# Optimization experiments

Hardware: AMD Instinct MI355X
Metric: run time of the kernel (lower is better)

Reference implementation:

```python
import jax, jax.numpy as jnp
import numpy as np

K = 64


def setup_inputs() -> dict:
    key = jax.random.key(0)
    k1, k2, k3, k4, k5 = jax.random.split(key, 5)
    B, D, F = 8192, 2048, 16384
    x = jax.random.normal(k1, (B, D), dtype=jnp.float32)
    W_enc = jax.random.normal(k2, (D, F), dtype=jnp.float32) * (1.0 / np.sqrt(D))
    b_enc = jax.random.normal(k3, (F,), dtype=jnp.float32) * 0.01
    W_dec = jax.random.normal(k4, (F, D), dtype=jnp.float32) * (1.0 / np.sqrt(F))
    b_dec = jax.random.normal(k5, (D,), dtype=jnp.float32) * 0.01
    return {"x": x, "W_enc": W_enc, "b_enc": b_enc, "W_dec": W_dec, "b_dec": b_dec}


def reference(x, W_enc, b_enc, W_dec, b_dec):
    # encode: dense GEMM + bias + relu -> [B, F]
    z = jax.nn.relu(x @ W_enc + b_enc)
    # top-k masking: keep only the k largest activations per row
    vals, idx = jax.lax.top_k(z, K)                     # [B, K]
    B = z.shape[0]
    rows = jnp.arange(B)[:, None]                       # [B, 1]
    sparse_z = jnp.zeros_like(z).at[rows, idx].set(vals)  # scatter back to [B, F]
    # decode: GEMM on k-sparse activations + bias -> [B, D]
    recon = sparse_z @ W_dec + b_dec
    return recon
```

## Files before the change

kernel.cpp:

```cpp
#include <hip/hip_runtime.h>
#include <hip/hip_bf16.h>
#include <stdint.h>

#define TK 64
#define FDIM 16384
#define DDIM 2048
#define NCAP 128
#define CCAP 384
#define SLOTS 12
#define TCAND 2.25f

typedef __attribute__((ext_vector_type(8))) short bf16x8;
typedef __attribute__((ext_vector_type(4))) float f32x4;

#define GLL(g, p)                                                        \
  __builtin_amdgcn_global_load_lds(                                      \
      (const __attribute__((address_space(1))) uint32_t*)(g),            \
      (__attribute__((address_space(3))) uint32_t*)(p), 16, 0, 0)

__device__ __forceinline__ unsigned short f2bf(float a) {
  union { float f; uint32_t u; } p; p.f = a;
  uint32_t u = p.u;
  return (unsigned short)((u + 0x7FFFu + ((u >> 16) & 1u)) >> 16);
}
__device__ __forceinline__ float bf2f(unsigned short h) {
  union { uint32_t u; float f; } p; p.u = ((uint32_t)h) << 16; return p.f;
}

__global__ __launch_bounds__(256) void conv_x(
    const float* __restrict__ x, unsigned short* __restrict__ xh, int n4)
{
  int i = blockIdx.x * 256 + threadIdx.x;
  const int stride = gridDim.x * 256;
  for (; i < n4; i += stride) {
    float4 v = ((const float4*)x)[i];
    ushort4 h;
    h.x = f2bf(v.x); h.y = f2bf(v.y); h.z = f2bf(v.z); h.w = f2bf(v.w);
    ((ushort4*)xh)[i] = h;
  }
}

__global__ __launch_bounds__(256) void conv_w(
    const float* __restrict__ W, float* __restrict__ wtf,
    unsigned short* __restrict__ wh)
{
  __shared__ float t[32][33];
  const int f0 = blockIdx.x * 32, d0 = blockIdx.y * 32;
  const int tr = threadIdx.x >> 3;
  const int tc = (threadIdx.x & 7) * 4;
  float4 v = *(const float4*)(W + (size_t)(d0 + tr) * FDIM + f0 + tc);
  t[tr][tc + 0] = v.x; t[tr][tc + 1] = v.y;
  t[tr][tc + 2] = v.z; t[tr][tc + 3] = v.w;
  __syncthreads();
  float a0 = t[tc + 0][tr], a1 = t[tc + 1][tr];
  float a2 = t[tc + 2][tr], a3 = t[tc + 3][tr];
  *(float4*)(wtf + (size_t)(f0 + tr) * DDIM + d0 + tc) =
      make_float4(a0, a1, a2, a3);
  ushort4 h;
  h.x = f2bf(a0); h.y = f2bf(a1); h.z = f2bf(a2); h.w = f2bf(a3);
  *(ushort4*)(wh + (size_t)(f0 + tr) * DDIM + d0 + tc) = h;
}

__global__ __launch_bounds__(256) void conv_wd(
    const float* __restrict__ W, unsigned short* __restrict__ Wb, int n4)
{
  int i = blockIdx.x * 256 + threadIdx.x;
  const int stride = gridDim.x * 256;
  for (; i < n4; i += stride) {
    float4 v = ((const float4*)W)[i];
    ushort4 h;
    h.x = f2bf(v.x); h.y = f2bf(v.y); h.z = f2bf(v.z); h.w = f2bf(v.w);
    ((ushort4*)Wb)[i] = h;
  }
}

__global__ __launch_bounds__(256) void enc_gemm_bf16(
    const unsigned short* __restrict__ xh,
    const unsigned short* __restrict__ wh,
    const float* __restrict__ bias,
    unsigned char* __restrict__ counts,
    uint2* __restrict__ slots,
    int B)
{
  __shared__ __align__(16) char smem[16384];
  const int tid = threadIdx.x;
  const int l = tid & 63;
  const int w = tid >> 6;
  const int wm = w >> 1, wn = w & 1;

  const int nbx = gridDim.x;
  const int nby = gridDim.y;
  const int lin = blockIdx.y * nbx + blockIdx.x;
  const int nwg = nbx * nby;
  const int cpx = nwg >> 3;
  const int swz = (lin & 7) * cpx + (lin >> 3);
  const int pstripe = 8 * nby;
  const int p  = swz / pstripe;
  const int rm = swz % pstripe;
  const int r  = rm >> 3;
  const int ci = rm & 7;
  const int row0 = r * 128;
  const int col0 = (p * 8 + ci) * 128;
  const int cb   = col0 >> 7;

  f32x4 acc[4][4] = {};

  const int sr = tid >> 2;
  const int sg = (tid & 3) ^ ((sr >> 1) & 3);
  const char* gxh = (const char*)xh + (size_t)row0 * 4096 + sg * 16;
  const char* gwh = (const char*)wh + (size_t)col0 * 4096 + sg * 16;

  const int lb = (l & 15) * 64 + (((l >> 4) ^ ((l >> 1) & 3)) << 4);
  const int aoff = wm * 4096 + lb;
  const int boff = 8192 + wn * 4096 + lb;

  for (int k0 = 0; k0 < DDIM; k0 += 32) {
    __syncthreads();
    const size_t kb = (size_t)k0 * 2;
#pragma unroll
    for (int i = 0; i < 2; ++i) {
      const size_t ro = (size_t)(i * 64 + sr) * 4096 + kb;
      char* lp = smem + i * 4096 + w * 1024;
      GLL(gxh + ro, lp);
      GLL(gwh + ro, lp + 8192);
    }
    __syncthreads();

    bf16x8 ah[4], bh[4];
#pragma unroll
    for (int f = 0; f < 4; ++f) {
      ah[f] = *(const bf16x8*)(smem + aoff + f * 1024);
      bh[f] = *(const bf16x8*)(smem + boff + f * 1024);
    }
#pragma unroll
    for (int fm = 0; fm < 4; ++fm)
#pragma unroll
      for (int fn = 0; fn < 4; ++fn)
        acc[fm][fn] = __builtin_amdgcn_mfma_f32_16x16x32_bf16(
            ah[fm], bh[fn], acc[fm][fn], 0, 0, 0);
  }

  __syncthreads();
  uint32_t* rcnt = (uint32_t*)smem;
  if (tid < 128) rcnt[tid] = 0;
  __syncthreads();

#pragma unroll
  for (int fn = 0; fn < 4; ++fn) {
    const int col = col0 + wn * 64 + fn * 16 + (l & 15);
    const float bb = bias[col];
#pragma unroll
    for (int fm = 0; fm < 4; ++fm) {
#pragma unroll
      for (int q = 0; q < 4; ++q) {
        const float zf = acc[fm][fn][q] + bb;
        if (zf > TCAND) {
          const int lr = wm * 64 + fm * 16 + (l >> 4) * 4 + q;
          const uint32_t pслot = atomicAdd(&rcnt[lr], 1u);
          if (pслot < SLOTS) {
            const size_t rz = (size_t)(row0 + lr);
            uint2 rec; rec.x = (uint32_t)col; rec.y = __float_as_uint(zf);
            slots[(rz * 128 + cb) * SLOTS + pслot] = rec;
          }
        }
      }
    }
  }
  __syncthreads();
  if (tid < 128) {
    uint32_t c = rcnt[tid];
    counts[(size_t)cb * B + row0 + tid] = (unsigned char)(c > 255u ? 255u : c);
  }
}

__global__ __launch_bounds__(256) void topk_kernel(
    const unsigned char* __restrict__ countsG,
    const uint2* __restrict__ slotsG,
    const float* __restrict__ x,
    const float* __restrict__ wtf,
    const float* __restrict__ benc,
    int*   __restrict__ outIdx,
    float* __restrict__ outVal,
    int B)
{
  const int row = blockIdx.x;
  const int tid = threadIdx.x;
  const float* xr = x + (size_t)row * DDIM;
  const uint2* slotsRow = slotsG + (size_t)row * 128 * SLOTS;

  __shared__ int    cnts[128];
  __shared__ int    sSum, sMax;
  __shared__ int    cIdx[CCAP];
  __shared__ float  cVal[CCAP];
  __shared__ short  sRank[CCAP];
  __shared__ unsigned char selF[CCAP];
  __shared__ int    cnt;
  __shared__ float  sV64;
  __shared__ int    wList[NCAP];
  __shared__ int    nW, winSel;
  __shared__ double dVals[NCAP];
  __shared__ int    keepFlag[NCAP];
  __shared__ double dred[256];

  if (tid == 0) { sSum = 0; sMax = 0; }
  __syncthreads();
  if (tid < 128) {
    int c = countsG[(size_t)tid * B + row];
    cnts[tid] = c;
    atomicAdd(&sSum, c);
    atomicMax(&sMax, c);
  }
  __syncthreads();
  const int total = sSum;
  bool useSlots = (total >= TK) && (total <= CCAP) && (sMax <= SLOTS);
  float Tlow = TCAND;
  int nc = 0;

  for (int pass = 0; pass < 2; ++pass) {
    if (tid == 0) cnt = 0;
    __syncthreads();
    if (useSlots) {
      for (int s = tid; s < 128 * SLOTS; s += 256) {
        const int cb = s / SLOTS, sl = s - cb * SLOTS;
        if (sl < cnts[cb]) {
          uint2 rec = slotsRow[s];
          int p = atomicAdd(&cnt, 1);
          cIdx[p] = (int)rec.x;
          cVal[p] = __uint_as_float(rec.y);
        }
      }
      __syncthreads();
      nc = cnt;
      __syncthreads();
    } else {
      float Tloc = Tlow;
      for (int attempt = 0; attempt < 16; ++attempt) {
        if (tid == 0) cnt = 0;
        __syncthreads();
        for (int f = tid; f < FDIM; f += 256) {
          const float* wr = wtf + (size_t)f * DDIM;
          float s = 0.f;
          for (int k = 0; k < DDIM; ++k) s = fmaf(xr[k], wr[k], s);
          const float zv = fmaxf(s + benc[f], 0.f);
          if (zv > Tloc) {
            int p = atomicAdd(&cnt, 1);
            if (p < CCAP) { cIdx[p] = f; cVal[p] = zv; }
          }
        }
        __syncthreads();
        nc = cnt;
        __syncthreads();
        if (nc >= TK && nc <= CCAP) break;
        Tloc += (nc > CCAP) ? 0.2f : -0.2f;
      }
      if (nc > CCAP) nc = CCAP;
    }

    for (int c = tid; c < nc; c += 256) {
      const float vi = cVal[c];
      const int   ii = cIdx[c];
      int rk = 0;
      for (int j = 0; j < nc; ++j) {
        const float vj = cVal[j];
        rk += (vj > vi) || (vj == vi && cIdx[j] < ii);
      }
      sRank[c] = (short)rk;
      selF[c] = (rk < TK) ? 1 : 0;
      if (rk == TK - 1) sV64 = vi;
    }
    __syncthreads();

    if (useSlots && sV64 - 0.02f <= TCAND) {
      useSlots = false;
      Tlow = sV64 - 0.04f;
      __syncthreads();
      continue;
    }
    break;
  }

  const float v64 = sV64;
  const float M = 0.02f;

  if (tid == 0) { nW = 0; winSel = 0; }
  __syncthreads();
  for (int c = tid; c < nc; c += 256) {
    if (fabsf(cVal[c] - v64) <= M) {
      int p = atomicAdd(&nW, 1);
      if (p < NCAP) wList[p] = c;
      if (sRank[c] < TK) atomicAdd(&winSel, 1);
    }
  }
  __syncthreads();
  const int nw = (nW < NCAP) ? nW : NCAP;

  if (nw > winSel) {
    for (int c = 0; c < nw; ++c) {
      const int f = cIdx[wList[c]];
      const float* wr = wtf + (size_t)f * DDIM;
      double part = 0.0;
      for (int k = tid; k < DDIM; k += 256)
        part += (double)xr[k] * (double)wr[k];
      dred[tid] = part;
      __syncthreads();
      for (int s = 128; s > 0; s >>= 1) {
        if (tid < s) dred[tid] += dred[tid + s];
        __syncthreads();
      }
      if (tid == 0) dVals[c] = dred[0] + (double)benc[f];
      __syncthreads();
    }
    if (tid == 0) {
      for (int c = 0; c < nw; ++c) keepFlag[c] = 0;
      int take = winSel < nw ? winSel : nw;
      for (int t = 0; t < take; ++t) {
        int best = -1;
        for (int c = 0; c < nw; ++c) {
          if (keepFlag[c]) continue;
          if (best < 0 || dVals[c] > dVals[best] ||
              (dVals[c] == dVals[best] && cIdx[wList[c]] < cIdx[wList[best]]))
            best = c;
        }
        keepFlag[best] = 1;
      }
      for (int c = 0; c < nw; ++c) selF[wList[c]] = (unsigned char)keepFlag[c];
    }
    __syncthreads();
  }

  for (int c = tid; c < nc; c += 256) {
    if (selF[c]) {
      const int myIdx = cIdx[c];
      int pos = 0;
      for (int j = 0; j < nc; ++j)
        pos += (selF[j] && cIdx[j] < myIdx);
      outIdx[(size_t)row * TK + pos] = myIdx;
      outVal[(size_t)row * TK + pos] = cVal[c];
    }
  }
}

__global__ __launch_bounds__(128) void decode_kernel(
    const int*   __restrict__ idxL,
    const float* __restrict__ valL,
    const unsigned short* __restrict__ Wdb,
    const float* __restrict__ bd,
    float* __restrict__ out,
    int nrows)
{
  const unsigned bid = blockIdx.x;
  const int slice = bid / (unsigned)nrows;
  const int row   = bid % (unsigned)nrows;
  const int tid = threadIdx.x;
  const int d = slice * 128 + tid;

  __shared__ int   si[TK];
  __shared__ float sv[TK];
  if (tid < TK) {
    si[tid] = idxL[(size_t)row * TK + tid];
    sv[tid] = valL[(size_t)row * TK + tid];
  }
  __syncthreads();

  float a = bd[d];
#pragma unroll 8
  for (int t = 0; t < TK; ++t)
    a = fmaf(sv[t], bf2f(Wdb[(size_t)si[t] * DDIM + d]), a);
  out[(size_t)row * DDIM + d] = a;
}

extern "C" void kernel_launch(void* const* d_in, const int* in_sizes, int n_in,
                              void* d_out, int out_size, void* d_ws, size_t ws_size,
                              hipStream_t stream) {
  const float* x    = (const float*)d_in[0];
  const float* Wenc = (const float*)d_in[1];
  const float* benc = (const float*)d_in[2];
  const float* Wdec = (const float*)d_in[3];
  const float* bdec = (const float*)d_in[4];
  float* out = (float*)d_out;

  const int D = in_sizes[4];
  const int B = in_sizes[0] / D;

  char* ws = (char*)d_ws;
  size_t off = 0;
  int*   idxL = (int*)ws;            off += (size_t)B * TK * 4;
  float* valL = (float*)(ws + off);  off += (size_t)B * TK * 4;
  off = (off + 255) & ~(size_t)255;
  float*          wtf = (float*)(ws + off);          off += (size_t)FDIM * DDIM * 4;
  unsigned short* wth = (unsigned short*)(ws + off); off += (size_t)FDIM * DDIM * 2;
  unsigned short* xh  = (unsigned short*)(ws + off); off += (size_t)B * DDIM * 2;
  unsigned short* wdb = (unsigned short*)(ws + off); off += (size_t)FDIM * DDIM * 2;
  off = (off + 255) & ~(size_t)255;
  unsigned char*  cntG = (unsigned char*)(ws + off); off += (size_t)128 * B;
  off = (off + 255) & ~(size_t)255;
  uint2*          slots = (uint2*)(ws + off);        off += (size_t)B * 128 * SLOTS * 8;

  conv_x<<<1024, 256, 0, stream>>>(x, xh, B * D / 4);
  conv_w<<<dim3(FDIM / 32, DDIM / 32), 256, 0, stream>>>(Wenc, wtf, wth);
  conv_wd<<<2048, 256, 0, stream>>>(Wdec, wdb, FDIM * DDIM / 4);

  dim3 g(FDIM / 128, B / 128);
  enc_gemm_bf16<<<g, 256, 0, stream>>>(xh, wth, benc, cntG, slots, B);
  topk_kernel<<<B, 256, 0, stream>>>(cntG, slots, x, wtf, benc,
                                     idxL, valL, B);
  decode_kernel<<<(DDIM / 128) * B, 128, 0, stream>>>(
      idxL, valL, wdb, bdec, out, B);
}
```

Baseline: 1.328 ms.

## Restructure encoder GEMM into 256x256 tiles with 4-stage async LDS pipeline

Encoder GEMM blocks grow from 128x128/256 threads to 256x256/512 threads, so each wave now computes an 8x4 grid of MFMA fragments. The single-buffered loop, which had a syncthreads on each side of every load, is replaced by a 4-buffer global_load_lds ring with explicit vmcnt waits that prefetches three K-steps ahead. The MFMA section runs at raised wave priority. The epilogue splits per-row candidate counters into two 128-column halves so the counts and slots layout that topk consumes stays the same. The aim is more data reuse and latency hiding in the dominant GEMM, at the cost of 128KB of LDS per block and higher register pressure.

```diff
diff --git a/kernel.cpp b/kernel.cpp
--- a/kernel.cpp
+++ b/kernel.cpp
@@ -74,7 +74,40 @@
   }
 }
 
-__global__ __launch_bounds__(256) void enc_gemm_bf16(
+#define STAGE(T) do {                                                        \
+    const int rb_ = (T) & 3;                                                 \
+    const size_t ko_ = (size_t)(T) * 64;                                     \
+    const size_t rA0 = (size_t)(row0 + sr4) * 4096 + ko_ + sgo;              \
+    GLL(gx + rA0, smem + rb_ * 32768 + wq);                                  \
+    const size_t rB0 = (size_t)(col0 + sr4) * 4096 + ko_ + sgo;              \
+    GLL(gw + rB0, smem + rb_ * 32768 + 16384 + wq);                          \
+    const size_t rA1 = (size_t)(row0 + 128 + sr4) * 4096 + ko_ + sgo;        \
+    GLL(gx + rA1, smem + rb_ * 32768 + 8192 + wq);                           \
+    const size_t rB1 = (size_t)(col0 + 128 + sr4) * 4096 + ko_ + sgo;        \
+    GLL(gw + rB1, smem + rb_ * 32768 + 16384 + 8192 + wq);                   \
+  } while (0)
+
+#define KSTEP(S, VMC, DOSTAGE) do {                                          \
+    asm volatile("s_waitcnt vmcnt(" #VMC ")" ::: "memory");                  \
+    __builtin_amdgcn_s_barrier();                                            \
+    const char* tb_ = smem + ((S) & 3) * 32768;                              \
+    bf16x8 af[8], bg[4];                                                     \
+    _Pragma("unroll") for (int m = 0; m < 8; ++m)                            \
+      af[m] = *(const bf16x8*)(tb_ + awm + m * 1024 + lb);                   \
+    _Pragma("unroll") for (int n = 0; n < 4; ++n)                            \
+      bg[n] = *(const bf16x8*)(tb_ + 16384 + bwn + n * 1024 + lb);           \
+    if (DOSTAGE) STAGE((S) + 3);                                             \
+    asm volatile("s_waitcnt lgkmcnt(0)" ::: "memory");                       \
+    __builtin_amdgcn_sched_barrier(0);                                       \
+    __builtin_amdgcn_s_setprio(1);                                           \
+    _Pragma("unroll") for (int m = 0; m < 8; ++m)                            \
+      _Pragma("unroll") for (int n = 0; n < 4; ++n)                          \
+        acc[m][n] = __builtin_amdgcn_mfma_f32_16x16x32_bf16(                 \
+            af[m], bg[n], acc[m][n], 0, 0, 0);                               \
+    __builtin_amdgcn_s_setprio(0);                                           \
+  } while (0)
+
+__global__ __launch_bounds__(512, 2) void enc_gemm_bf16(
     const unsigned short* __restrict__ xh,
     const unsigned short* __restrict__ wh,
     const float* __restrict__ bias,
@@ -82,11 +115,11 @@
     uint2* __restrict__ slots,
     int B)
 {
-  __shared__ __align__(16) char smem[16384];
+  __shared__ __align__(16) char smem[131072];
   const int tid = threadIdx.x;
   const int l = tid & 63;
   const int w = tid >> 6;
-  const int wm = w >> 1, wn = w & 1;
+  const int wm = w >> 2, wn = w & 3;
 
   const int nbx = gridDim.x;
   const int nby = gridDim.y;
@@ -94,82 +127,65 @@
   const int nwg = nbx * nby;
   const int cpx = nwg >> 3;
   const int swz = (lin & 7) * cpx + (lin >> 3);
-  const int pstripe = 8 * nby;
+  const int pstripe = 2 * nby;
   const int p  = swz / pstripe;
   const int rm = swz % pstripe;
-  const int r  = rm >> 3;
-  const int ci = rm & 7;
-  const int row0 = r * 128;
-  const int col0 = (p * 8 + ci) * 128;
-  const int cb   = col0 >> 7;
-
-  f32x4 acc[4][4] = {};
-
-  const int sr = tid >> 2;
-  const int sg = (tid & 3) ^ ((sr >> 1) & 3);
-  const char* gxh = (const char*)xh + (size_t)row0 * 4096 + sg * 16;
-  const char* gwh = (const char*)wh + (size_t)col0 * 4096 + sg * 16;
-
-  const int lb = (l & 15) * 64 + (((l >> 4) ^ ((l >> 1) & 3)) << 4);
-  const int aoff = wm * 4096 + lb;
-  const int boff = 8192 + wn * 4096 + lb;
-
-  for (int k0 = 0; k0 < DDIM; k0 += 32) {
-    __syncthreads();
-    const size_t kb = (size_t)k0 * 2;
+  const int row0 = (rm >> 1) * 256;
+  const int col0 = (p * 2 + (rm & 1)) * 256;
+
+  f32x4 acc[8][4] = {};
+
+  const int sr4 = tid >> 2;
+  const int sg  = (tid & 3) ^ ((sr4 >> 1) & 3);
+  const size_t sgo = (size_t)sg * 16;
+  const int wq = w * 1024;
+  const char* gx = (const char*)xh;
+  const char* gw = (const char*)wh;
+
+  const int lb  = (l & 15) * 64 + (((l >> 4) ^ ((l >> 1) & 3)) << 4);
+  const int awm = wm * 8192;
+  const int bwn = wn * 4096;
+
+  STAGE(0); STAGE(1); STAGE(2);
+
+  for (int s = 0; s < 61; ++s) KSTEP(s, 8, 1);
+  KSTEP(61, 8, 0);
+  KSTEP(62, 4, 0);
+  KSTEP(63, 0, 0);
+
+  __syncthreads();
+  uint32_t* rcnt = (uint32_t*)smem;
+  rcnt[tid] = 0;
+  __syncthreads();
+
 #pragma unroll
-    for (int i = 0; i < 2; ++i) {
-      const size_t ro = (size_t)(i * 64 + sr) * 4096 + kb;
-      char* lp = smem + i * 4096 + w * 1024;
-      GLL(gxh + ro, lp);
-      GLL(gwh + ro, lp + 8192);
-    }
-    __syncthreads();
-
-    bf16x8 ah[4], bh[4];
+  for (int n = 0; n < 4; ++n) {
+    const int col = col0 + wn * 64 + n * 16 + (l & 15);
+    const float bb = bias[col];
+    const int half = wn >> 1;
 #pragma unroll
-    for (int f = 0; f < 4; ++f) {
-      ah[f] = *(const bf16x8*)(smem + aoff + f * 1024);
-      bh[f] = *(const bf16x8*)(smem + boff + f * 1024);
-    }
-#pragma unroll
-    for (int fm = 0; fm < 4; ++fm)
-#pragma unroll
-      for (int fn = 0; fn < 4; ++fn)
-        acc[fm][fn] = __builtin_amdgcn_mfma_f32_16x16x32_bf16(
-            ah[fm], bh[fn], acc[fm][fn], 0, 0, 0);
-  }
-
-  __syncthreads();
-  uint32_t* rcnt = (uint32_t*)smem;
-  if (tid < 128) rcnt[tid] = 0;
-  __syncthreads();
-
-#pragma unroll
-  for (int fn = 0; fn < 4; ++fn) {
-    const int col = col0 + wn * 64 + fn * 16 + (l & 15);
-    const float bb = bias[col];
-#pragma unroll
-    for (int fm = 0; fm < 4; ++fm) {
+    for (int m = 0; m < 8; ++m) {
 #pragma unroll
       for (int q = 0; q < 4; ++q) {
-        const float zf = acc[fm][fn][q] + bb;
+        const float zf = acc[m][n][q] + bb;
         if (zf > TCAND) {
-          const int lr = wm * 64 + fm * 16 + (l >> 4) * 4 + q;
-          const uint32_t pслot = atomicAdd(&rcnt[lr], 1u);
-          if (pслot < SLOTS) {
-            const size_t rz = (size_t)(row0 + lr);
+          const int lr = wm * 128 + m * 16 + (l >> 4) * 4 + q;
+          const uint32_t ps = atomicAdd(&rcnt[lr * 2 + half], 1u);
+          if (ps < SLOTS) {
             uint2 rec; rec.x = (uint32_t)col; rec.y = __float_as_uint(zf);
-            slots[(rz * 128 + cb) * SLOTS + pслot] = rec;
+            slots[((size_t)(row0 + lr) * 128 + (col0 >> 7) + half) * SLOTS + ps]
+                = rec;
           }
         }
       }
     }
   }
   __syncthreads();
-  if (tid < 128) {
+  {
+    const int lr = tid >> 1, half = tid & 1;
     uint32_t c = rcnt[tid];
-    counts[(size_t)cb * B + row0 + tid] = (unsigned char)(c > 255u ? 255u : c);
+    counts[(size_t)((col0 >> 7) + half) * B + row0 + lr] =
+        (unsigned char)(c > 255u ? 255u : c);
   }
 }
 
@@ -400,8 +416,8 @@
   conv_w<<<dim3(FDIM / 32, DDIM / 32), 256, 0, stream>>>(Wenc, wtf, wth);
   conv_wd<<<2048, 256, 0, stream>>>(Wdec, wdb, FDIM * DDIM / 4);
 
-  dim3 g(FDIM / 128, B / 128);
-  enc_gemm_bf16<<<g, 256, 0, stream>>>(xh, wth, benc, cntG, slots, B);
+  dim3 g(FDIM / 256, B / 256);
+  enc_gemm_bf16<<<g, 512, 0, stream>>>(xh, wth, benc, cntG, slots, B);
   topk_kernel<<<B, 256, 0, stream>>>(cntG, slots, x, wtf, benc,
                                      idxL, valL, B);
   decode_kernel<<<(DDIM / 128) * B, 128, 0, stream>>>(
```

New measurement: 1.216 ms. 1.09x faster.
